# Kernel optimization log

Hardware: AMD Instinct MI355X
Metric: run time of the kernel (lower is better)

## Reference

```python
import jax, jax.numpy as jnp
import numpy as np

M, K, CH = 4, 256, 256
D = CH // M  # per-group dim = 64


def _conv(x, w, b, stride=2):
    # x: [N,C,H,W], w: [O,I,kh,kw]
    y = jax.lax.conv_general_dilated(
        x, w, window_strides=(stride, stride), padding='SAME',
        dimension_numbers=('NCHW', 'OIHW', 'NCHW'))
    return y + b[None, :, None, None]


def _encoder(x, w1, b1, w2, b2, w3, b3, w4, b4):
    x = jax.nn.gelu(_conv(x, w1, b1))
    x = jax.nn.gelu(_conv(x, w2, b2))
    x = jax.nn.gelu(_conv(x, w3, b3))
    return _conv(x, w4, b4)


def setup_inputs() -> dict:
    key = jax.random.key(0)
    ks = jax.random.split(key, 12)
    x = jax.random.uniform(ks[0], (16, 3, 256, 256), jnp.float32)

    def w(k, shape, fan_in):
        return jax.random.normal(k, shape, jnp.float32) * (1.0 / np.sqrt(fan_in))

    w1 = w(ks[1], (64, 3, 3, 3), 3 * 9);    b1 = jnp.zeros((64,), jnp.float32)
    w2 = w(ks[2], (128, 64, 3, 3), 64 * 9); b2 = jnp.zeros((128,), jnp.float32)
    w3 = w(ks[3], (256, 128, 3, 3), 128 * 9); b3 = jnp.zeros((256,), jnp.float32)
    w4 = w(ks[4], (CH, 256, 3, 3), 256 * 9); b4 = jnp.zeros((CH,), jnp.float32)
    codebook = w(ks[5], (M, K, D), D)
    wq = w(ks[6], (M, D, D), D)
    wk = w(ks[7], (M, D, D), D)
    return dict(x=x, w1=w1, b1=b1, w2=w2, b2=b2, w3=w3, b3=b3, w4=w4, b4=b4,
                codebook=codebook, wq=wq, wk=wk)


def reference(x, w1, b1, w2, b2, w3, b3, w4, b4, codebook, wq, wk):
    x = (x - 0.5) / 0.5
    n, c, h, w = x.shape  # c == 3 here, so the c==1 expand branch is skipped
    hPad = max(0, 32 - h)
    wPad = max(0, 32 - w)
    if hPad or wPad:
        x = jnp.pad(x, ((0, 0), (0, 0), (0, hPad), (0, wPad)))
    latent = _encoder(x, w1, b1, w2, b2, w3, b3, w4, b4)  # [n, CH, h/16, w/16]
    n2, _, hh, ww = latent.shape
    q = latent.transpose(0, 2, 3, 1).reshape(n2, hh, ww, M, D)
    q = jnp.einsum('nhwmd,mcd->nhwmc', q, wq)            # per-group query proj
    kproj = jnp.einsum('mkd,mcd->mkc', codebook, wk)     # per-group key proj
    scores = jnp.einsum('nhwmd,mkd->nhwmk', q, kproj)    # [n,hh,ww,m,k]
    code = jnp.argmax(scores, axis=-1).astype(jnp.uint8)
    return code, jnp.array([h, w], dtype=jnp.int32)
```

## Files before the change

kernel.cpp:

```cpp
#include <hip/hip_runtime.h>
#include <math.h>


typedef _Float16 half8 __attribute__((ext_vector_type(8)));
typedef float floatx4 __attribute__((ext_vector_type(4)));
typedef unsigned int u32;
typedef unsigned short u16;

__device__ __forceinline__ float gelu_tanh(float x) {
    float x3 = x * x * x;
    float t = 1.5957691216057308f * x + 0.07135481627333636f * x3;
    return x / (1.0f + __expf(-t));
}

__device__ __forceinline__ u32 pack_split(float v) {
    _Float16 h = (_Float16)v;
    _Float16 l = (_Float16)((v - (float)h) * 4096.0f);
    union { _Float16 f; u16 s; } a, b;
    a.f = h; b.f = l;
    return (u32)a.s | ((u32)b.s << 16);
}

template <int Ci, int Co>
__global__ void prep_w(const float* __restrict__ W, _Float16* __restrict__ dH,
                       _Float16* __restrict__ dL) {
    constexpr int KC = Ci / 32, NTg = Co / 16;
    int lin = blockIdx.x * 256 + threadIdx.x;
    if (lin >= 9 * KC * NTg * 64) return;
    int l = lin & 63;
    int q = lin >> 6;
    int nt = q % NTg; q /= NTg;
    int kc = q % KC;
    int tap = q / KC;
    int co = nt * 16 + (l & 15);
    int ci0 = kc * 32 + ((l >> 4) << 3);
#pragma unroll
    for (int j = 0; j < 8; ++j) {
        float v = W[((size_t)co * Ci + ci0 + j) * 9 + tap];
        _Float16 h = (_Float16)v;
        _Float16 lo = (_Float16)((v - (float)h) * 4096.0f);
        dH[(size_t)lin * 8 + j] = h;
        dL[(size_t)lin * 8 + j] = lo;
    }
}

__launch_bounds__(256)
__global__ void conv1_k(const float* __restrict__ x, const float* __restrict__ w,
                        const float* __restrict__ bias, u32* __restrict__ out) {
    __shared__ float win[17 * 260];
    __shared__ float wsh[27 * 64];
    const int t = threadIdx.x;
    const int tx = t & 15, ty = (t >> 4) & 7, cz = t >> 7;
    int bx = blockIdx.x;
    const int cg = bx & 3;
    const int oyt = (bx >> 2) & 15;
    const int n = bx >> 6;
    const int co0 = cg * 16 + cz * 8;
    const int oy = oyt * 8 + ty;
    const int ox0 = tx * 8;
    const int iy0 = oyt * 16;

    for (int e = t; e < 27 * 64; e += 256) {
        int co = e & 63, ct = e >> 6;
        wsh[ct * 64 + co] = w[co * 27 + ct];
    }

    float acc[8][8];
#pragma unroll
    for (int c = 0; c < 8; ++c)
#pragma unroll
        for (int p = 0; p < 8; ++p) acc[c][p] = 0.0f;

    for (int ci = 0; ci < 3; ++ci) {
        __syncthreads();
        for (int e = t; e < 17 * 65; e += 256) {
            int r = e / 65, c4 = (e - r * 65) * 4;
            int iy = iy0 + r;
            float4 v = {0.0f, 0.0f, 0.0f, 0.0f};
            if (c4 < 256 && iy < 256) {
                float4 g = *(const float4*)&x[((size_t)(n * 3 + ci) * 256 + iy) * 256 + c4];
                v.x = 2.0f * g.x - 1.0f; v.y = 2.0f * g.y - 1.0f;
                v.z = 2.0f * g.z - 1.0f; v.w = 2.0f * g.w - 1.0f;
            }
            *(float4*)&win[r * 260 + c4] = v;
        }
        __syncthreads();

#pragma unroll
        for (int ky = 0; ky < 3; ++ky) {
            const float* rowp = &win[(2 * ty + ky) * 260 + 16 * tx];
            float rv[20];
#pragma unroll
            for (int q = 0; q < 5; ++q) {
                float4 v4 = *(const float4*)(rowp + 4 * q);
                rv[4 * q + 0] = v4.x; rv[4 * q + 1] = v4.y;
                rv[4 * q + 2] = v4.z; rv[4 * q + 3] = v4.w;
            }
#pragma unroll
            for (int kx = 0; kx < 3; ++kx) {
                const float* wp = &wsh[(ci * 9 + ky * 3 + kx) * 64 + co0];
                float wv[8];
#pragma unroll
                for (int q = 0; q < 2; ++q) {
                    float4 v4 = *(const float4*)(wp + 4 * q);
                    wv[4 * q + 0] = v4.x; wv[4 * q + 1] = v4.y;
                    wv[4 * q + 2] = v4.z; wv[4 * q + 3] = v4.w;
                }
#pragma unroll
                for (int c = 0; c < 8; ++c)
#pragma unroll
                    for (int p = 0; p < 8; ++p)
                        acc[c][p] += rv[2 * p + kx] * wv[c];
            }
        }
    }

    float bj[8];
#pragma unroll
    for (int c = 0; c < 8; ++c) bj[c] = bias[co0 + c];
#pragma unroll
    for (int p = 0; p < 8; ++p) {
        int ox = ox0 + p;
        size_t base = ((size_t)(n * 128 + oy) * 128 + ox) * 64 + co0;
        uint4 s0, s1;
        s0.x = pack_split(gelu_tanh(acc[0][p] + bj[0]));
        s0.y = pack_split(gelu_tanh(acc[1][p] + bj[1]));
        s0.z = pack_split(gelu_tanh(acc[2][p] + bj[2]));
        s0.w = pack_split(gelu_tanh(acc[3][p] + bj[3]));
        s1.x = pack_split(gelu_tanh(acc[4][p] + bj[4]));
        s1.y = pack_split(gelu_tanh(acc[5][p] + bj[5]));
        s1.z = pack_split(gelu_tanh(acc[6][p] + bj[6]));
        s1.w = pack_split(gelu_tanh(acc[7][p] + bj[7]));
        *(uint4*)&out[base] = s0;
        *(uint4*)&out[base + 4] = s1;
    }
}

template <int Ci, int Co, int Hi, int Wi, int NWAVE, bool GELU, bool SPLIT>
__launch_bounds__(NWAVE * 64)
__global__ void conv_mfma(const u32* __restrict__ in, const _Float16* __restrict__ WbH,
                          const _Float16* __restrict__ WbL, const float* __restrict__ bias,
                          void* __restrict__ outp) {
    constexpr int Ho = Hi / 2, Wo = Wi / 2;
    constexpr int KC = Ci / 32, NTg = Co / 16;
    constexpr int OYT = Ho / 4, OXT = Wo / 16, CGT = Co / (16 * NWAVE);
    constexpr int WC = 33, CIBP = 40;
    constexpr int NT = NWAVE * 64;
    __shared__ _Float16 AH[9 * WC * CIBP], AL[9 * WC * CIBP];

    const int t = threadIdx.x, l = t & 63, wid = t >> 6;
    const int wm = wid / (NWAVE / 2), wn = wid % (NWAVE / 2);
    int bx = blockIdx.x;
    const int cg = bx % CGT;  bx /= CGT;
    const int oxt = bx % OXT; bx /= OXT;
    const int oyt = bx % OYT; bx /= OYT;
    const int n = bx;
    const int oy0 = oyt * 4, ox0 = oxt * 16, co0 = cg * 16 * NWAVE, nt0 = co0 >> 4;
    const int iy0 = oy0 * 2, ix0 = ox0 * 2;

    floatx4 aM[2][2], aX[2][2];
    floatx4 zz = {0.0f, 0.0f, 0.0f, 0.0f};
#pragma unroll
    for (int a = 0; a < 2; ++a)
#pragma unroll
        for (int b = 0; b < 2; ++b) { aM[a][b] = zz; aX[a][b] = zz; }

    const int bfrag = (wn * 2) * 512 + l * 8;

    for (int kc = 0; kc < KC; ++kc) {
        __syncthreads();
        for (int e = t; e < 9 * WC * 4; e += NT) {
            int og = e & 3, px = e >> 2;
            int r = px / WC, cx = px - r * WC;
            int iy = iy0 + r, ix = ix0 + cx;
            union { float4 f4[2]; u32 u[8]; } buf;
            if (iy < Hi && ix < Wi) {
                const float4* g = (const float4*)(in + (((size_t)(n * Hi + iy) * Wi + ix) * Ci + kc * 32 + og * 8));
                buf.f4[0] = g[0]; buf.f4[1] = g[1];
            } else {
#pragma unroll
                for (int k2 = 0; k2 < 8; ++k2) buf.u[k2] = 0;
            }
            union { float4 f4; u16 s[8]; } hh, ll;
#pragma unroll
            for (int k2 = 0; k2 < 8; ++k2) {
                hh.s[k2] = (u16)buf.u[k2];
                ll.s[k2] = (u16)(buf.u[k2] >> 16);
            }
            int off = px * CIBP + og * 8;
            *(float4*)&AH[off] = hh.f4;
            *(float4*)&AL[off] = ll.f4;
        }
        __syncthreads();

#pragma unroll
        for (int tap = 0; tap < 9; ++tap) {
            const size_t src = ((size_t)(tap * KC + kc) * NTg + nt0) * 512 + bfrag;
            half8 bh[2], bl[2];
#pragma unroll
            for (int b = 0; b < 2; ++b) {
                bh[b] = *(const half8*)&WbH[src + b * 512];
                bl[b] = *(const half8*)&WbL[src + b * 512];
            }
            const int ky = tap / 3, kx = tap - ky * 3;
#pragma unroll
            for (int a = 0; a < 2; ++a) {
                int mt = wm * 2 + a;
                int off = ((2 * mt + ky) * WC + 2 * (l & 15) + kx) * CIBP + (l >> 4) * 8;
                half8 ah = *(half8*)&AH[off];
                half8 al = *(half8*)&AL[off];
#pragma unroll
                for (int b = 0; b < 2; ++b) {
                    aM[a][b] = __builtin_amdgcn_mfma_f32_16x16x32_f16(ah, bh[b], aM[a][b], 0, 0, 0);
                    aX[a][b] = __builtin_amdgcn_mfma_f32_16x16x32_f16(ah, bl[b], aX[a][b], 0, 0, 0);
                    aX[a][b] = __builtin_amdgcn_mfma_f32_16x16x32_f16(al, bh[b], aX[a][b], 0, 0, 0);
                }
            }
        }
    }

#pragma unroll
    for (int a = 0; a < 2; ++a) {
        int oy = oy0 + wm * 2 + a;
#pragma unroll
        for (int b = 0; b < 2; ++b) {
            int co = co0 + (wn * 2 + b) * 16 + (l & 15);
            float bj = bias[co];
#pragma unroll
            for (int r = 0; r < 4; ++r) {
                int ox = ox0 + (l >> 4) * 4 + r;
                float v = aM[a][b][r] + aX[a][b][r] * (1.0f / 4096.0f) + bj;
                if (GELU) v = gelu_tanh(v);
                size_t oidx = ((size_t)(n * Ho + oy) * Wo + ox) * Co + co;
                if (SPLIT) ((u32*)outp)[oidx] = pack_split(v);
                else       ((float*)outp)[oidx] = v;
            }
        }
    }
}

__global__ void kproj_kernel(const float* __restrict__ cb,
                             const float* __restrict__ wk,
                             float* __restrict__ kp) {
    int m = blockIdx.x >> 8;
    int k = blockIdx.x & 255;
    int c = threadIdx.x;
    const float* cbp = cb + (size_t)(m * 256 + k) * 64;
    const float* wkp = wk + (size_t)(m * 64 + c) * 64;
    float acc = 0.0f;
#pragma unroll 8
    for (int d = 0; d < 64; ++d) acc += cbp[d] * wkp[d];
    kp[(size_t)(m * 256 + k) * 64 + c] = acc;
}

__global__ void m_kernel(const float* __restrict__ wq,
                         const float* __restrict__ kp,
                         float* __restrict__ M) {
    int m = blockIdx.x >> 8;
    int k = blockIdx.x & 255;
    int d = threadIdx.x;
    const float* kpp = &kp[(size_t)(m * 256 + k) * 64];
    const float* wqp = &wq[(size_t)m * 64 * 64 + d];
    float acc = 0.0f;
#pragma unroll 8
    for (int c = 0; c < 64; ++c) acc += wqp[c * 64] * kpp[c];
    M[((size_t)(m * 256 + k)) * 64 + d] = acc;
}

__launch_bounds__(256)
__global__ void head_kernel(const float* __restrict__ latent,
                            const float* __restrict__ M,
                            int* __restrict__ out) {
    __shared__ float rs[256];
    __shared__ int rk[256];
    const int t = threadIdx.x;
    const int px = t & 15, m = (t >> 4) & 3, kq = t >> 6;
    const int pix = blockIdx.x * 16 + px;

    float4 lr[16];
    const float4* lp = (const float4*)&latent[(size_t)pix * 256 + m * 64];
#pragma unroll
    for (int d = 0; d < 16; ++d) lr[d] = lp[d];

    float best = -INFINITY;
    int bestk = 0;
    const float4* Mp = (const float4*)&M[(size_t)((m * 256 + kq * 64)) * 64];
    for (int kk = 0; kk < 64; ++kk) {
        float s0 = 0.0f, s1 = 0.0f, s2 = 0.0f, s3 = 0.0f;
#pragma unroll
        for (int d = 0; d < 16; ++d) {
            float4 mv = Mp[kk * 16 + d];
            s0 += lr[d].x * mv.x; s1 += lr[d].y * mv.y;
            s2 += lr[d].z * mv.z; s3 += lr[d].w * mv.w;
        }
        float s = (s0 + s1) + (s2 + s3);
        if (s > best) { best = s; bestk = kq * 64 + kk; }
    }
    rs[t] = best; rk[t] = bestk;
    __syncthreads();
    if (kq == 0) {
#pragma unroll
        for (int q = 1; q < 4; ++q) {
            float sv = rs[t + 64 * q];
            int kv = rk[t + 64 * q];
            if (sv > best || (sv == best && kv < bestk)) { best = sv; bestk = kv; }
        }
        out[pix * 4 + m] = bestk;
    }
    if (blockIdx.x == 0 && t == 0) { out[16384] = 256; out[16385] = 256; }
}

extern "C" void kernel_launch(void* const* d_in, const int* in_sizes, int n_in,
                              void* d_out, int out_size, void* d_ws, size_t ws_size,
                              hipStream_t stream) {
    const float* x  = (const float*)d_in[0];
    const float* w1 = (const float*)d_in[1];  const float* b1 = (const float*)d_in[2];
    const float* w2 = (const float*)d_in[3];  const float* b2 = (const float*)d_in[4];
    const float* w3 = (const float*)d_in[5];  const float* b3 = (const float*)d_in[6];
    const float* w4 = (const float*)d_in[7];  const float* b4 = (const float*)d_in[8];
    const float* cb = (const float*)d_in[9];
    const float* wq = (const float*)d_in[10];
    const float* wk = (const float*)d_in[11];
    int* out = (int*)d_out;

    char* ws = (char*)d_ws;
    u32*   buf1 = (u32*)ws;
    u32*   buf2 = (u32*)(ws + 67108864);
    u32*   buf3 = (u32*)(ws + 100663296);
    float* buf4 = (float*)(ws + 117440512);
    float* kp   = (float*)(ws + 121634816);
    float* Mbuf = (float*)(ws + 121634816 + 262144);

    _Float16* w2H = (_Float16*)(ws + 100663296);
    _Float16* w2L = w2H + 9 * 2 * 8 * 512;
    _Float16* w3H = (_Float16*)ws;
    _Float16* w3L = w3H + 9 * 4 * 16 * 512;
    _Float16* w4H = w3L + 9 * 4 * 16 * 512;
    _Float16* w4L = w4H + 9 * 8 * 16 * 512;

    prep_w<64, 128><<<36, 256, 0, stream>>>(w2, w2H, w2L);
    conv1_k<<<1024, 256, 0, stream>>>(x, w1, b1, buf1);
    conv_mfma<64, 128, 128, 128, 8, true, true><<<1024, 512, 0, stream>>>(buf1, w2H, w2L, b2, buf2);
    prep_w<128, 256><<<144, 256, 0, stream>>>(w3, w3H, w3L);
    prep_w<256, 256><<<288, 256, 0, stream>>>(w4, w4H, w4L);
    conv_mfma<128, 256, 64, 64, 8, true, true><<<512, 512, 0, stream>>>(buf2, w3H, w3L, b3, buf3);
    kproj_kernel<<<4 * 256, 64, 0, stream>>>(cb, wk, kp);
    m_kernel<<<4 * 256, 64, 0, stream>>>(wq, kp, Mbuf);
    conv_mfma<256, 256, 32, 32, 4, false, false><<<256, 256, 0, stream>>>(buf3, w4H, w4L, b4, buf4);
    head_kernel<<<256, 256, 0, stream>>>(buf4, Mbuf, out);
}
```

Baseline: 299.6 us.

## Split-K the final conv across four blocks and add a partial-sum reduce kernel

The last conv layer previously launched only 256 blocks, which underfills the GPU. It now splits the input-channel loop four ways, giving 1024 blocks that each write fp32 partial sums to a workspace region. A new reduce kernel sums the four partials and adds the bias. The trade-off is extra global traffic for the partial buffers, one more kernel launch, and a changed floating-point summation order.

After: 284.1 us. -5.2%, faster.

```diff
diff --git a/kernel.cpp b/kernel.cpp
--- a/kernel.cpp
+++ b/kernel.cpp
@@ -136,7 +136,7 @@
     }
 }
 
-template <int Ci, int Co, int Hi, int Wi, int NWAVE, bool GELU, bool SPLIT>
+template <int Ci, int Co, int Hi, int Wi, int NWAVE, int KSPLIT, bool GELU, bool SPLIT>
 __launch_bounds__(NWAVE * 64)
 __global__ void conv_mfma(const u32* __restrict__ in, const _Float16* __restrict__ WbH,
                           const _Float16* __restrict__ WbL, const float* __restrict__ bias,
@@ -146,11 +146,13 @@
     constexpr int OYT = Ho / 4, OXT = Wo / 16, CGT = Co / (16 * NWAVE);
     constexpr int WC = 33, CIBP = 40;
     constexpr int NT = NWAVE * 64;
+    constexpr int KCS = KC / KSPLIT;
     __shared__ _Float16 AH[9 * WC * CIBP], AL[9 * WC * CIBP];
 
     const int t = threadIdx.x, l = t & 63, wid = t >> 6;
     const int wm = wid / (NWAVE / 2), wn = wid % (NWAVE / 2);
     int bx = blockIdx.x;
+    const int ks = bx % KSPLIT;  bx /= KSPLIT;
     const int cg = bx % CGT;  bx /= CGT;
     const int oxt = bx % OXT; bx /= OXT;
     const int oyt = bx % OYT; bx /= OYT;
@@ -167,7 +169,7 @@
 
     const int bfrag = (wn * 2) * 512 + l * 8;
 
-    for (int kc = 0; kc < KC; ++kc) {
+    for (int kc = ks * KCS; kc < (ks + 1) * KCS; ++kc) {
         __syncthreads();
         for (int e = t; e < 9 * WC * 4; e += NT) {
             int og = e & 3, px = e >> 2;
@@ -225,18 +227,40 @@
 #pragma unroll
         for (int b = 0; b < 2; ++b) {
             int co = co0 + (wn * 2 + b) * 16 + (l & 15);
-            float bj = bias[co];
+            float bj = (KSPLIT == 1) ? bias[co] : 0.0f;
 #pragma unroll
             for (int r = 0; r < 4; ++r) {
                 int ox = ox0 + (l >> 4) * 4 + r;
                 float v = aM[a][b][r] + aX[a][b][r] * (1.0f / 4096.0f) + bj;
-                if (GELU) v = gelu_tanh(v);
                 size_t oidx = ((size_t)(n * Ho + oy) * Wo + ox) * Co + co;
-                if (SPLIT) ((u32*)outp)[oidx] = pack_split(v);
-                else       ((float*)outp)[oidx] = v;
-            }
-        }
-    }
+                if (KSPLIT > 1) {
+                    ((float*)outp)[(size_t)ks * (16 * Ho * Wo * Co) + oidx] = v;
+                } else {
+                    if (GELU) v = gelu_tanh(v);
+                    if (SPLIT) ((u32*)outp)[oidx] = pack_split(v);
+                    else       ((float*)outp)[oidx] = v;
+                }
+            }
+        }
+    }
+}
+
+__global__ void reduce4_k(const float* __restrict__ part,
+                          const float* __restrict__ bias,
+                          float* __restrict__ out) {
+    constexpr int PS4 = 16 * 16 * 16 * 256 / 4;
+    int gid = blockIdx.x * 256 + threadIdx.x;
+    const float4* p = (const float4*)part;
+    float4 s = p[gid];
+    float4 q1 = p[PS4 + gid];
+    float4 q2 = p[2 * PS4 + gid];
+    float4 q3 = p[3 * PS4 + gid];
+    s.x += q1.x; s.y += q1.y; s.z += q1.z; s.w += q1.w;
+    s.x += q2.x; s.y += q2.y; s.z += q2.z; s.w += q2.w;
+    s.x += q3.x; s.y += q3.y; s.z += q3.z; s.w += q3.w;
+    float4 b = *(const float4*)&bias[(gid * 4) & 255];
+    s.x += b.x; s.y += b.y; s.z += b.z; s.w += b.w;
+    ((float4*)out)[gid] = s;
 }
 
 __global__ void kproj_kernel(const float* __restrict__ cb,
@@ -337,15 +361,17 @@
     _Float16* w3L = w3H + 9 * 4 * 16 * 512;
     _Float16* w4H = w3L + 9 * 4 * 16 * 512;
     _Float16* w4L = w4H + 9 * 8 * 16 * 512;
+    float* part4 = (float*)(ws + 67108864);
 
     prep_w<64, 128><<<36, 256, 0, stream>>>(w2, w2H, w2L);
     conv1_k<<<1024, 256, 0, stream>>>(x, w1, b1, buf1);
-    conv_mfma<64, 128, 128, 128, 8, true, true><<<1024, 512, 0, stream>>>(buf1, w2H, w2L, b2, buf2);
+    conv_mfma<64, 128, 128, 128, 8, 1, true, true><<<1024, 512, 0, stream>>>(buf1, w2H, w2L, b2, buf2);
     prep_w<128, 256><<<144, 256, 0, stream>>>(w3, w3H, w3L);
     prep_w<256, 256><<<288, 256, 0, stream>>>(w4, w4H, w4L);
-    conv_mfma<128, 256, 64, 64, 8, true, true><<<512, 512, 0, stream>>>(buf2, w3H, w3L, b3, buf3);
+    conv_mfma<128, 256, 64, 64, 8, 1, true, true><<<512, 512, 0, stream>>>(buf2, w3H, w3L, b3, buf3);
     kproj_kernel<<<4 * 256, 64, 0, stream>>>(cb, wk, kp);
     m_kernel<<<4 * 256, 64, 0, stream>>>(wq, kp, Mbuf);
-    conv_mfma<256, 256, 32, 32, 4, false, false><<<256, 256, 0, stream>>>(buf3, w4H, w4L, b4, buf4);
+    conv_mfma<256, 256, 32, 32, 4, 4, false, false><<<1024, 256, 0, stream>>>(buf3, w4H, w4L, b4, part4);
+    reduce4_k<<<1024, 256, 0, stream>>>(part4, b4, buf4);
     head_kernel<<<256, 256, 0, stream>>>(buf4, Mbuf, out);
 }
```
